# Kernel tuning notes

Measured on AMD Instinct MI355X. Metric: run time of the kernel, lower is better.

Reference implementation:

```python
import jax, jax.numpy as jnp
import numpy as np

N = 100000      # points
M = 12500       # cluster centers
E0 = 1600000    # point-level edges
E1 = 400000     # cluster-level edges
F_IN = 4        # raw point feature dim (e.g. intensity + extras)
D = 64          # hidden feature width
N_CLASSES = 8


def setup_inputs() -> dict:
    key = jax.random.key(0)
    ks = jax.random.split(key, 20)
    s = 0.05
    d = {}
    d["features"] = jax.random.normal(ks[0], (N, F_IN), jnp.float32)
    d["points"] = jax.random.normal(ks[1], (N, 3), jnp.float32)
    d["cluster_centers"] = jax.random.normal(ks[2], (M, 3), jnp.float32)
    d["l0_edges"] = jax.random.randint(ks[3], (E0, 2), 0, N)
    d["l1_edges"] = jax.random.randint(ks[4], (E1, 2), 0, M)
    d["labels"] = jax.random.randint(ks[5], (N,), 0, M)
    # Feature_extract MLP
    d["W_fe"] = s * jax.random.normal(ks[6], (F_IN + 3, D), jnp.float32)
    d["b_fe"] = jnp.zeros((D,), jnp.float32)
    # 4 Mini_GNN layers (layer2, layer2_1, layer6, layer6_1), stacked
    d["mini_We"] = s * jax.random.normal(ks[7], (4, D + 3, D), jnp.float32)
    d["mini_be"] = jnp.zeros((4, D), jnp.float32)
    d["mini_Wu"] = s * jax.random.normal(ks[8], (4, D, D), jnp.float32)
    d["mini_bu"] = jnp.zeros((4, D), jnp.float32)
    # Mini_to_Large
    d["W_m1"] = s * jax.random.normal(ks[9], (D + 3, D), jnp.float32)
    d["b_m1"] = jnp.zeros((D,), jnp.float32)
    d["W_m2"] = s * jax.random.normal(ks[10], (D, D), jnp.float32)
    d["b_m2"] = jnp.zeros((D,), jnp.float32)
    # 2 GNN layers on cluster graph (layer4, layer4_1), stacked
    d["gnn_We"] = s * jax.random.normal(ks[11], (2, D + 3, D), jnp.float32)
    d["gnn_be"] = jnp.zeros((2, D), jnp.float32)
    d["gnn_Wu"] = s * jax.random.normal(ks[12], (2, D, D), jnp.float32)
    d["gnn_bu"] = jnp.zeros((2, D), jnp.float32)
    # Large_to_Mini
    d["W_l"] = s * jax.random.normal(ks[13], (D + 3, D), jnp.float32)
    d["b_l"] = jnp.zeros((D,), jnp.float32)
    # Classifier
    d["W_c"] = s * jax.random.normal(ks[14], (D, N_CLASSES), jnp.float32)
    d["b_c"] = jnp.zeros((N_CLASSES,), jnp.float32)
    return d


def _gnn_layer(feat, pos, edges, We, be, Wu, bu, n_nodes):
    """PointGNN-style layer: gather -> edge MLP -> scatter max -> update MLP -> residual."""
    src, dst = edges[:, 0], edges[:, 1]
    e_in = jnp.concatenate([pos[src] - pos[dst], feat[src]], axis=-1)  # [E, 3+D]
    h = jax.nn.relu(e_in @ We + be)                                     # [E, D]
    agg = jax.ops.segment_max(h, dst, num_segments=n_nodes)            # [n, D]
    agg = jnp.where(jnp.isneginf(agg), 0.0, agg)  # nodes with no in-edges -> 0
    return jax.nn.relu(agg @ Wu + bu) + feat


def reference(features, points, cluster_centers, l0_edges, l1_edges, labels,
              W_fe, b_fe, mini_We, mini_be, mini_Wu, mini_bu,
              W_m1, b_m1, W_m2, b_m2, gnn_We, gnn_be, gnn_Wu, gnn_bu,
              W_l, b_l, W_c, b_c):
    rel = points - cluster_centers[labels]  # [N, 3] point pos relative to its cluster
    # layer1: Feature_extract
    f1 = jax.nn.relu(jnp.concatenate([features, rel], -1) @ W_fe + b_fe)
    # layer2 / layer2_1: Mini_GNN (scatter max) on point graph
    f2 = _gnn_layer(f1, points, l0_edges, mini_We[0], mini_be[0], mini_Wu[0], mini_bu[0], N)
    f2_1 = _gnn_layer(f2, points, l0_edges, mini_We[1], mini_be[1], mini_Wu[1], mini_bu[1], N)
    # layer3: Mini_to_Large (scatter sum by labels)
    h = jax.nn.relu(jnp.concatenate([f2_1, rel], -1) @ W_m1 + b_m1)
    c = jax.ops.segment_sum(h, labels, num_segments=M)  # [M, D]
    f3 = jax.nn.relu(c @ W_m2 + b_m2)
    # layer4 / layer4_1: GNN (scatter max) on cluster graph
    f4 = _gnn_layer(f3, cluster_centers, l1_edges, gnn_We[0], gnn_be[0], gnn_Wu[0], gnn_bu[0], M)
    f4_1 = _gnn_layer(f4, cluster_centers, l1_edges, gnn_We[1], gnn_be[1], gnn_Wu[1], gnn_bu[1], M)
    # layer5: Large_to_Mini (gather by labels)
    f5 = jax.nn.relu(jnp.concatenate([f4_1[labels], rel], -1) @ W_l + b_l)
    # layer6 / layer6_1 with residual skips per call()
    f6 = _gnn_layer(f5, points, l0_edges, mini_We[2], mini_be[2], mini_Wu[2], mini_bu[2], N)
    f6 = f6 + f2_1
    f6_1 = _gnn_layer(f6, points, l0_edges, mini_We[3], mini_be[3], mini_Wu[3], mini_bu[3], N)
    final = f6_1 + f2
    return final @ W_c + b_c  # [N, N_CLASSES] per-point logits
```

## Files before the change

### kernel.cpp

```cpp
#include <hip/hip_runtime.h>

#define N_PTS   100000
#define M_CL    12500
#define E0_N    1600000
#define E1_N    400000

#define NB      256
#define BIN_CAP 32
#define RANGE0  391
#define RANGE1  49
#define BCAP0   8192
#define BCAP1   2048

#define LSTR    72

typedef unsigned short ushortT;
typedef short  short8 __attribute__((ext_vector_type(8)));
typedef float  v4f    __attribute__((ext_vector_type(4)));
typedef _Float16 h2   __attribute__((ext_vector_type(2)));
typedef unsigned u4v  __attribute__((ext_vector_type(4)));

__device__ inline ushortT f2bf(float x){
  union{float f; unsigned u;} v; v.f = x;
  unsigned r = v.u + 0x7fffu + ((v.u >> 16) & 1u);
  return (ushortT)(r >> 16);
}
__device__ inline float bf2f(ushortT h){
  union{unsigned u; float f;} v; v.u = ((unsigned)h) << 16;
  return v.f;
}
__device__ inline ushortT f2h(float x){
  union{_Float16 h; ushortT u;} v; v.h = (_Float16)x;
  return v.u;
}
__device__ inline float h2f(ushortT u){
  union{ushortT u; _Float16 h;} v; v.u = u;
  return (float)v.h;
}
__device__ inline h2 pkmax(h2 a, h2 b){ return __builtin_elementwise_max(a, b); }
__device__ inline h2 u2h(unsigned u){ union{unsigned u; h2 h;} v{u}; return v.h; }


__global__ void k_binit(int* c0, int* c1){
  int t = threadIdx.x;
  c0[t] = t*BCAP0;
  c1[t] = t*BCAP1;
}

template<int RANGE>
__global__ __launch_bounds__(256) void k_bin(const int* __restrict__ edges, int E,
                                             int* __restrict__ bcur, unsigned* __restrict__ tmp){
  __shared__ unsigned stage[NB*BIN_CAP];
  __shared__ int scnt[NB];
  __shared__ int sbase[NB];
  int tid = threadIdx.x;
  int nchunks = (E + 2047) / 2048;
  for (int c = blockIdx.x; c < nchunks; c += gridDim.x){
    int base = c*2048;
    scnt[tid] = 0;
    __syncthreads();
    #pragma unroll
    for (int r=0;r<8;++r){
      int e = base + r*256 + tid;
      if (e < E){
        int s = edges[2*e], d = edges[2*e+1];
        int bk = d / RANGE;
        unsigned packed = ((unsigned)s << 11) | (unsigned)(d - bk*RANGE);
        int pos = atomicAdd(&scnt[bk], 1);
        if (pos < BIN_CAP) stage[bk*BIN_CAP+pos] = packed;
        else tmp[atomicAdd(&bcur[bk],1)] = packed;
      }
    }
    __syncthreads();
    {
      int nfl = scnt[tid]; if (nfl > BIN_CAP) nfl = BIN_CAP;
      sbase[tid] = atomicAdd(&bcur[tid], nfl);
    }
    __syncthreads();
    int wv = tid >> 6, ln = tid & 63;
    for (int bb=0; bb<32; ++bb){
      int bk = wv*64 + bb*2 + (ln>>5);
      int ent = ln & 31;
      int nf = scnt[bk]; if (nf > BIN_CAP) nf = BIN_CAP;
      if (ent < nf) tmp[sbase[bk]+ent] = stage[bk*BIN_CAP+ent];
    }
    __syncthreads();
  }
}

__global__ void k_scan_bases(const int* c0, int* bb0, int* off0e,
                             const int* c1, int* bb1, int* off1e){
  const int* cur = blockIdx.x ? c1 : c0;
  int* bb = blockIdx.x ? bb1 : bb0;
  int* offe = blockIdx.x ? off1e : off0e;
  int BC = blockIdx.x ? BCAP1 : BCAP0;
  int lane = threadIdx.x & 63;
  int base = lane*4;
  int v0 = cur[base+0] - (base+0)*BC;
  int v1 = cur[base+1] - (base+1)*BC;
  int v2 = cur[base+2] - (base+2)*BC;
  int v3 = cur[base+3] - (base+3)*BC;
  int psum = v0+v1+v2+v3, sc = psum;
  #pragma unroll
  for (int st=1; st<64; st<<=1){
    int x = __shfl_up(sc, st, 64);
    if (lane >= st) sc += x;
  }
  int ex = sc - psum;
  bb[base+0] = ex;
  bb[base+1] = ex + v0;
  bb[base+2] = ex + v0 + v1;
  bb[base+3] = ex + v0 + v1 + v2;
  if (lane == 63) *offe = sc;
}

template<int RANGE, int BCAP>
__global__ __launch_bounds__(256) void k_csr_build(const unsigned* __restrict__ tmp, const int* __restrict__ bcur,
                                                   const int* __restrict__ bb, int n,
                                                   int* __restrict__ offs, int* __restrict__ csr){
  constexpr int K = (RANGE + 255) / 256;
  __shared__ int hist[RANGE];
  __shared__ int part[256];
  int b = blockIdx.x, tid = threadIdx.x;
  int dlo = b*RANGE;
  int range = n - dlo; if (range > RANGE) range = RANGE; if (range < 0) range = 0;
  int cnt = bcur[b] - b*BCAP;
  for (int t=tid; t<RANGE; t+=256) hist[t] = 0;
  __syncthreads();
  const unsigned* sl = tmp + (size_t)b*BCAP;
  for (int j=tid; j<cnt; j+=256) atomicAdd(&hist[sl[j] & 2047u], 1);
  __syncthreads();
  int s = 0; int loc[K];
  #pragma unroll
  for (int kk=0; kk<K; ++kk){
    int idx = tid*K + kk;
    int v = (idx < RANGE) ? hist[idx] : 0;
    loc[kk] = s; s += v;
  }
  part[tid] = s; __syncthreads();
  int own = s;
  for (int st=1; st<256; st<<=1){
    int x = (tid >= st) ? part[tid-st] : 0;
    __syncthreads();
    part[tid] += x;
    __syncthreads();
  }
  int ebase = part[tid] - own;
  int gb = bb[b];
  __syncthreads();
  #pragma unroll
  for (int kk=0; kk<K; ++kk){
    int idx = tid*K + kk;
    if (idx < RANGE){
      int ex = ebase + loc[kk];
      if (idx < range) offs[dlo+idx] = gb + ex;
      hist[idx] = ex;
    }
  }
  __syncthreads();
  for (int j=tid; j<cnt; j+=256){
    unsigned p = sl[j];
    int pos = atomicAdd(&hist[p & 2047u], 1);
    csr[gb + pos] = (int)(p >> 11);
  }
}


__global__ __launch_bounds__(256) void k_count_lab(const int* __restrict__ labels, int n, int* __restrict__ cnt){
  int i = blockIdx.x*256 + threadIdx.x;
  if (i < n) atomicAdd(&cnt[labels[i]], 1);
}

__global__ __launch_bounds__(256) void k_chunk_sum(const int* __restrict__ cnt, int n, int* __restrict__ part){
  __shared__ int sd[256];
  int t = threadIdx.x, base = blockIdx.x*2048;
  int s = 0;
  #pragma unroll
  for (int r=0;r<8;++r){ int i = base + t*8 + r; if (i<n) s += cnt[i]; }
  sd[t]=s; __syncthreads();
  for (int st=128; st>0; st>>=1){ if (t<st) sd[t]+=sd[t+st]; __syncthreads(); }
  if (t==0) part[blockIdx.x]=sd[0];
}

__global__ void k_scan_part(int* part, int B, int* offs, int n){
  int lane = threadIdx.x & 63;
  int v = (lane < B) ? part[lane] : 0;
  int orig = v;
  #pragma unroll
  for (int st=1; st<64; st<<=1){
    int x = __shfl_up(v, st, 64);
    if (lane >= st) v += x;
  }
  if (lane < B) part[lane] = v - orig;
  if (lane == 63) offs[n] = v;
}

__global__ __launch_bounds__(256) void k_chunk_scan(const int* __restrict__ cnt, int n,
                                                    const int* __restrict__ part, int* __restrict__ offs){
  __shared__ int sd[256];
  int t=threadIdx.x, base=blockIdx.x*2048;
  int v[8]; int s=0;
  #pragma unroll
  for (int r=0;r<8;++r){ int i=base+t*8+r; v[r] = (i<n)?cnt[i]:0; s+=v[r]; }
  sd[t]=s; __syncthreads();
  for (int st=1; st<256; st<<=1){
    int x = (t>=st)? sd[t-st] : 0;
    __syncthreads();
    sd[t]+=x;
    __syncthreads();
  }
  int acc = part[blockIdx.x] + sd[t] - s;
  #pragma unroll
  for (int r=0;r<8;++r){ int i=base+t*8+r; if (i<n) offs[i]=acc; acc+=v[r]; }
}

__global__ __launch_bounds__(256) void k_fill_lab(const int* __restrict__ labels, int n,
                                                  const int* __restrict__ offs, int* __restrict__ cur,
                                                  int* __restrict__ csr){
  int i = blockIdx.x*256 + threadIdx.x;
  if (i < n){
    int d = labels[i];
    int p = atomicAdd(&cur[d], 1);
    csr[offs[d]+p] = i;
  }
}


struct WSrc { const float* p[16]; };

__global__ __launch_bounds__(256) void k_wprep(WSrc s, ushortT* __restrict__ wt, ushortT* __restrict__ wtc){
  int slot = blockIdx.x;
  if (slot < 15){
    const float* src = s.p[slot];
    ushortT* dst = wt + slot*4096;
    for (int e=threadIdx.x; e<4096; e+=256){
      int nn = e>>6, kk = e&63;
      dst[e] = f2bf(src[kk*64+nn]);
    }
  } else {
    const float* src = s.p[15];
    for (int e=threadIdx.x; e<1024; e+=256){
      int nn = e>>6, kk = e&63;
      wtc[e] = (nn<8) ? f2bf(src[kk*8+nn]) : (ushortT)0;
    }
  }
}


__global__ __launch_bounds__(256) void k_f1g(const float* __restrict__ features, const float* __restrict__ points,
                                             const float* __restrict__ centers, const int* __restrict__ labels,
                                             const float* __restrict__ W, const float* __restrict__ b,
                                             const ushortT* __restrict__ Wt2, const float* __restrict__ bias2,
                                             const float* __restrict__ Wr2,
                                             float* __restrict__ rel, ushortT* __restrict__ f1b,
                                             ushortT* __restrict__ gout, int n, int ntiles){
  __shared__ ushortT lds[4*16*LSTR];
  int tid = threadIdx.x;
  int lane = tid & 63, wslot = tid >> 6;
  int quad = lane >> 4, l15 = lane & 15;
  int gw = (blockIdx.x*256 + tid) >> 6;
  int nw = (gridDim.x*256) >> 6;
  float Wf0=W[0*64+lane], Wf1=W[1*64+lane], Wf2=W[2*64+lane], Wf3=W[3*64+lane];
  float wr0=W[4*64+lane], wr1=W[5*64+lane], wr2=W[6*64+lane];
  float bias=b[lane];
  short8 s0_0 = *(const short8*)(Wt2 + ( 0 + l15)*64 +  0 + quad*8);
  short8 s0_1 = *(const short8*)(Wt2 + ( 0 + l15)*64 + 32 + quad*8);
  short8 s1_0 = *(const short8*)(Wt2 + (16 + l15)*64 +  0 + quad*8);
  short8 s1_1 = *(const short8*)(Wt2 + (16 + l15)*64 + 32 + quad*8);
  short8 s2_0 = *(const short8*)(Wt2 + (32 + l15)*64 +  0 + quad*8);
  short8 s2_1 = *(const short8*)(Wt2 + (32 + l15)*64 + 32 + quad*8);
  short8 s3_0 = *(const short8*)(Wt2 + (48 + l15)*64 +  0 + quad*8);
  short8 s3_1 = *(const short8*)(Wt2 + (48 + l15)*64 + 32 + quad*8);
  float eb0 = bias2[l15], eb1 = bias2[16+l15], eb2 = bias2[32+l15], eb3 = bias2[48+l15];
  float e0c0=Wr2[0*64+l15], e0c1=Wr2[0*64+16+l15], e0c2=Wr2[0*64+32+l15], e0c3=Wr2[0*64+48+l15];
  float e1c0=Wr2[1*64+l15], e1c1=Wr2[1*64+16+l15], e1c2=Wr2[1*64+32+l15], e1c3=Wr2[1*64+48+l15];
  float e2c0=Wr2[2*64+l15], e2c1=Wr2[2*64+16+l15], e2c2=Wr2[2*64+32+l15], e2c3=Wr2[2*64+48+l15];

  for (int t=gw; t<ntiles; t+=nw){
    int i0 = t*16;
    for (int r=0;r<16;++r){
      int row = i0 + r;
      bool ok = row < n;
      int rr = ok ? row : n-1;
      int lb = labels[rr];
      float rx = points[rr*3+0]-centers[lb*3+0];
      float ry = points[rr*3+1]-centers[lb*3+1];
      float rz = points[rr*3+2]-centers[lb*3+2];
      float acc = bias + wr0*rx + wr1*ry + wr2*rz;
      acc += features[rr*4+0]*Wf0 + features[rr*4+1]*Wf1;
      acc += features[rr*4+2]*Wf2 + features[rr*4+3]*Wf3;
      acc = fmaxf(acc, 0.f);
      ushortT ab = f2bf(acc);
      if (ok){
        f1b[(size_t)row*64+lane] = ab;
        if (lane==0){ rel[row*3+0]=rx; rel[row*3+1]=ry; rel[row*3+2]=rz; }
      }
      lds[wslot*(16*LSTR) + r*LSTR + lane] = ab;
    }
    __builtin_amdgcn_wave_barrier();
    const ushortT* lp = lds + wslot*(16*LSTR) + l15*LSTR + quad*8;
    short8 sa0 = *(const short8*)(lp);
    short8 sa1 = *(const short8*)(lp + 32);
    __builtin_amdgcn_wave_barrier();
    v4f ec0 = {0.f,0.f,0.f,0.f}, ec1 = ec0, ec2 = ec0, ec3 = ec0;
    ec0 = __builtin_amdgcn_mfma_f32_16x16x32_bf16(sa0, s0_0, ec0, 0,0,0);
    ec1 = __builtin_amdgcn_mfma_f32_16x16x32_bf16(sa0, s1_0, ec1, 0,0,0);
    ec2 = __builtin_amdgcn_mfma_f32_16x16x32_bf16(sa0, s2_0, ec2, 0,0,0);
    ec3 = __builtin_amdgcn_mfma_f32_16x16x32_bf16(sa0, s3_0, ec3, 0,0,0);
    ec0 = __builtin_amdgcn_mfma_f32_16x16x32_bf16(sa1, s0_1, ec0, 0,0,0);
    ec1 = __builtin_amdgcn_mfma_f32_16x16x32_bf16(sa1, s1_1, ec1, 0,0,0);
    ec2 = __builtin_amdgcn_mfma_f32_16x16x32_bf16(sa1, s2_1, ec2, 0,0,0);
    ec3 = __builtin_amdgcn_mfma_f32_16x16x32_bf16(sa1, s3_1, ec3, 0,0,0);
    #pragma unroll
    for (int r=0;r<4;++r){
      int row = i0 + quad*4 + r;
      if (row < n){
        float vx=points[row*3+0], vy=points[row*3+1], vz=points[row*3+2];
        float g0 = ec0[r] + eb0 + vx*e0c0 + vy*e1c0 + vz*e2c0;
        float g1 = ec1[r] + eb1 + vx*e0c1 + vy*e1c1 + vz*e2c1;
        float g2 = ec2[r] + eb2 + vx*e0c2 + vy*e1c2 + vz*e2c2;
        float g3 = ec3[r] + eb3 + vx*e0c3 + vy*e1c3 + vz*e2c3;
        size_t base = (size_t)row*64 + l15;
        gout[base] = f2h(g0); gout[base+16] = f2h(g1); gout[base+32] = f2h(g2); gout[base+48] = f2h(g3);
      }
    }
  }
}


template<bool RELU, int NRES, bool USEREL, bool GATHER, bool OUT16, bool F16O, int EMODE, bool ERELU>
__global__ __launch_bounds__(256) void k_gemm(
    const ushortT* __restrict__ A, const ushortT* __restrict__ Wt,
    const float* __restrict__ bias, const float* __restrict__ Wr,
    const float* __restrict__ rel, const int* __restrict__ gidx,
    const ushortT* __restrict__ r1, const ushortT* __restrict__ r2,
    ushortT* __restrict__ out16,
    const ushortT* __restrict__ Wt2, const float* __restrict__ bias2,
    const float* __restrict__ Wr2, const float* __restrict__ vec2,
    void* __restrict__ eout,
    int n, int ntiles)
{
  constexpr int LDSZ = (EMODE>0) ? 4*16*LSTR : 4;
  __shared__ ushortT lds[LDSZ];
  int tid = threadIdx.x;
  int lane = tid & 63, wslot = tid >> 6;
  int quad = lane >> 4, l15 = lane & 15;
  int gw = (blockIdx.x*256 + tid) >> 6;
  int nw = (gridDim.x*256) >> 6;

  short8 bfr0_0 = *(const short8*)(Wt + ( 0 + l15)*64 +  0 + quad*8);
  short8 bfr0_1 = *(const short8*)(Wt + ( 0 + l15)*64 + 32 + quad*8);
  short8 bfr1_0 = *(const short8*)(Wt + (16 + l15)*64 +  0 + quad*8);
  short8 bfr1_1 = *(const short8*)(Wt + (16 + l15)*64 + 32 + quad*8);
  short8 bfr2_0 = *(const short8*)(Wt + (32 + l15)*64 +  0 + quad*8);
  short8 bfr2_1 = *(const short8*)(Wt + (32 + l15)*64 + 32 + quad*8);
  short8 bfr3_0 = *(const short8*)(Wt + (48 + l15)*64 +  0 + quad*8);
  short8 bfr3_1 = *(const short8*)(Wt + (48 + l15)*64 + 32 + quad*8);
  float bs0 = bias[ 0 + l15], bs1 = bias[16 + l15];
  float bs2 = bias[32 + l15], bs3 = bias[48 + l15];
  float w0c0=0,w0c1=0,w0c2=0,w0c3=0, w1c0=0,w1c1=0,w1c2=0,w1c3=0, w2c0=0,w2c1=0,w2c2=0,w2c3=0;
  if (USEREL){
    w0c0=Wr[0*64+l15]; w0c1=Wr[0*64+16+l15]; w0c2=Wr[0*64+32+l15]; w0c3=Wr[0*64+48+l15];
    w1c0=Wr[1*64+l15]; w1c1=Wr[1*64+16+l15]; w1c2=Wr[1*64+32+l15]; w1c3=Wr[1*64+48+l15];
    w2c0=Wr[2*64+l15]; w2c1=Wr[2*64+16+l15]; w2c2=Wr[2*64+32+l15]; w2c3=Wr[2*64+48+l15];
  }

  short8 s0_0{}, s0_1{}, s1_0{}, s1_1{}, s2_0{}, s2_1{}, s3_0{}, s3_1{};
  float eb0=0, eb1=0, eb2=0, eb3=0;
  float e0c0=0,e0c1=0,e0c2=0,e0c3=0, e1c0=0,e1c1=0,e1c2=0,e1c3=0, e2c0=0,e2c1=0,e2c2=0,e2c3=0;
  float ebias_c = 0.f;
  if (EMODE == 1){
    s0_0 = *(const short8*)(Wt2 + ( 0 + l15)*64 +  0 + quad*8);
    s0_1 = *(const short8*)(Wt2 + ( 0 + l15)*64 + 32 + quad*8);
    s1_0 = *(const short8*)(Wt2 + (16 + l15)*64 +  0 + quad*8);
    s1_1 = *(const short8*)(Wt2 + (16 + l15)*64 + 32 + quad*8);
    s2_0 = *(const short8*)(Wt2 + (32 + l15)*64 +  0 + quad*8);
    s2_1 = *(const short8*)(Wt2 + (32 + l15)*64 + 32 + quad*8);
    s3_0 = *(const short8*)(Wt2 + (48 + l15)*64 +  0 + quad*8);
    s3_1 = *(const short8*)(Wt2 + (48 + l15)*64 + 32 + quad*8);
    eb0 = bias2[l15]; eb1 = bias2[16+l15]; eb2 = bias2[32+l15]; eb3 = bias2[48+l15];
    e0c0=Wr2[0*64+l15]; e0c1=Wr2[0*64+16+l15]; e0c2=Wr2[0*64+32+l15]; e0c3=Wr2[0*64+48+l15];
    e1c0=Wr2[1*64+l15]; e1c1=Wr2[1*64+16+l15]; e1c2=Wr2[1*64+32+l15]; e1c3=Wr2[1*64+48+l15];
    e2c0=Wr2[2*64+l15]; e2c1=Wr2[2*64+16+l15]; e2c2=Wr2[2*64+32+l15]; e2c3=Wr2[2*64+48+l15];
  } else if (EMODE == 2){
    s0_0 = *(const short8*)(Wt2 + l15*64 +  0 + quad*8);
    s0_1 = *(const short8*)(Wt2 + l15*64 + 32 + quad*8);
    ebias_c = (l15 < 8) ? bias2[l15] : 0.f;
  }

  for (int t=gw; t<ntiles; t+=nw){
    int i0 = t*16;
    int rowA = i0 + l15; if (rowA >= n) rowA = n-1;
    if (GATHER) rowA = gidx[rowA];
    const ushortT* ap = A + (size_t)rowA*64 + quad*8;
    short8 a0 = *(const short8*)(ap);
    short8 a1 = *(const short8*)(ap + 32);
    v4f ac0 = {0.f,0.f,0.f,0.f}, ac1 = ac0, ac2 = ac0, ac3 = ac0;
    ac0 = __builtin_amdgcn_mfma_f32_16x16x32_bf16(a0, bfr0_0, ac0, 0,0,0);
    ac1 = __builtin_amdgcn_mfma_f32_16x16x32_bf16(a0, bfr1_0, ac1, 0,0,0);
    ac2 = __builtin_amdgcn_mfma_f32_16x16x32_bf16(a0, bfr2_0, ac2, 0,0,0);
    ac3 = __builtin_amdgcn_mfma_f32_16x16x32_bf16(a0, bfr3_0, ac3, 0,0,0);
    ac0 = __builtin_amdgcn_mfma_f32_16x16x32_bf16(a1, bfr0_1, ac0, 0,0,0);
    ac1 = __builtin_amdgcn_mfma_f32_16x16x32_bf16(a1, bfr1_1, ac1, 0,0,0);
    ac2 = __builtin_amdgcn_mfma_f32_16x16x32_bf16(a1, bfr2_1, ac2, 0,0,0);
    ac3 = __builtin_amdgcn_mfma_f32_16x16x32_bf16(a1, bfr3_1, ac3, 0,0,0);

    #pragma unroll
    for (int r=0;r<4;++r){
      int row = i0 + quad*4 + r;
      bool rowok = (row < n);
      float rx=0.f, ry=0.f, rz=0.f;
      if (USEREL && rowok){ rx=rel[row*3+0]; ry=rel[row*3+1]; rz=rel[row*3+2]; }
      float v0 = ac0[r] + bs0, v1 = ac1[r] + bs1, v2 = ac2[r] + bs2, v3 = ac3[r] + bs3;
      if (USEREL){
        v0 += rx*w0c0 + ry*w1c0 + rz*w2c0;
        v1 += rx*w0c1 + ry*w1c1 + rz*w2c1;
        v2 += rx*w0c2 + ry*w1c2 + rz*w2c2;
        v3 += rx*w0c3 + ry*w1c3 + rz*w2c3;
      }
      if (RELU){ v0=fmaxf(v0,0.f); v1=fmaxf(v1,0.f); v2=fmaxf(v2,0.f); v3=fmaxf(v3,0.f); }
      size_t base = (size_t)row*64 + l15;
      if (rowok){
        if (NRES>=1){
          v0 += bf2f(r1[base]); v1 += bf2f(r1[base+16]); v2 += bf2f(r1[base+32]); v3 += bf2f(r1[base+48]);
        }
        if (NRES>=2){
          v0 += bf2f(r2[base]); v1 += bf2f(r2[base+16]); v2 += bf2f(r2[base+32]); v3 += bf2f(r2[base+48]);
        }
        if (OUT16){
          if (F16O){
            out16[base] = f2h(v0); out16[base+16] = f2h(v1); out16[base+32] = f2h(v2); out16[base+48] = f2h(v3);
          } else {
            out16[base] = f2bf(v0); out16[base+16] = f2bf(v1); out16[base+32] = f2bf(v2); out16[base+48] = f2bf(v3);
          }
        }
      }
      if (EMODE > 0){
        int lb = wslot*(16*LSTR) + (quad*4+r)*LSTR + l15;
        lds[lb]      = f2bf(v0);
        lds[lb + 16] = f2bf(v1);
        lds[lb + 32] = f2bf(v2);
        lds[lb + 48] = f2bf(v3);
      }
    }

    if (EMODE > 0){
      __builtin_amdgcn_wave_barrier();
      const ushortT* lp = lds + wslot*(16*LSTR) + l15*LSTR + quad*8;
      short8 sa0 = *(const short8*)(lp);
      short8 sa1 = *(const short8*)(lp + 32);
      __builtin_amdgcn_wave_barrier();
      if (EMODE == 1){
        v4f ec0 = {0.f,0.f,0.f,0.f}, ec1 = ec0, ec2 = ec0, ec3 = ec0;
        ec0 = __builtin_amdgcn_mfma_f32_16x16x32_bf16(sa0, s0_0, ec0, 0,0,0);
        ec1 = __builtin_amdgcn_mfma_f32_16x16x32_bf16(sa0, s1_0, ec1, 0,0,0);
        ec2 = __builtin_amdgcn_mfma_f32_16x16x32_bf16(sa0, s2_0, ec2, 0,0,0);
        ec3 = __builtin_amdgcn_mfma_f32_16x16x32_bf16(sa0, s3_0, ec3, 0,0,0);
        ec0 = __builtin_amdgcn_mfma_f32_16x16x32_bf16(sa1, s0_1, ec0, 0,0,0);
        ec1 = __builtin_amdgcn_mfma_f32_16x16x32_bf16(sa1, s1_1, ec1, 0,0,0);
        ec2 = __builtin_amdgcn_mfma_f32_16x16x32_bf16(sa1, s2_1, ec2, 0,0,0);
        ec3 = __builtin_amdgcn_mfma_f32_16x16x32_bf16(sa1, s3_1, ec3, 0,0,0);
        ushortT* eo = (ushortT*)eout;
        #pragma unroll
        for (int r=0;r<4;++r){
          int row = i0 + quad*4 + r;
          if (row < n){
            float vx=vec2[row*3+0], vy=vec2[row*3+1], vz=vec2[row*3+2];
            float g0 = ec0[r] + eb0 + vx*e0c0 + vy*e1c0 + vz*e2c0;
            float g1 = ec1[r] + eb1 + vx*e0c1 + vy*e1c1 + vz*e2c1;
            float g2 = ec2[r] + eb2 + vx*e0c2 + vy*e1c2 + vz*e2c2;
            float g3 = ec3[r] + eb3 + vx*e0c3 + vy*e1c3 + vz*e2c3;
            if (ERELU){ g0=fmaxf(g0,0.f); g1=fmaxf(g1,0.f); g2=fmaxf(g2,0.f); g3=fmaxf(g3,0.f); }
            size_t base = (size_t)row*64 + l15;
            eo[base] = f2h(g0); eo[base+16] = f2h(g1); eo[base+32] = f2h(g2); eo[base+48] = f2h(g3);
          }
        }
      } else {
        v4f ec = {0.f,0.f,0.f,0.f};
        ec = __builtin_amdgcn_mfma_f32_16x16x32_bf16(sa0, s0_0, ec, 0,0,0);
        ec = __builtin_amdgcn_mfma_f32_16x16x32_bf16(sa1, s0_1, ec, 0,0,0);
        if (l15 < 8){
          float* eo = (float*)eout;
          #pragma unroll
          for (int r=0;r<4;++r){
            int row = i0 + quad*4 + r;
            if (row < n) eo[(size_t)row*8 + l15] = ec[r] + ebias_c;
          }
        }
      }
    }
  }
}


__global__ __launch_bounds__(256) void k_edge_agg(const int* __restrict__ offs, const int* __restrict__ csr,
                                                  const float* __restrict__ pos, const ushortT* __restrict__ g,
                                                  const float* __restrict__ Wp, ushortT* __restrict__ agg, int n){
  int lane = threadIdx.x & 63;
  int grp = lane >> 3, d8 = lane & 7;
  int gbase = lane & 56;
  int gw = (blockIdx.x*256 + threadIdx.x) >> 6;
  int nw = (gridDim.x*256) >> 6;
  const u4v* g4 = (const u4v*)g;
  float2 w0[4], w1[4], w2[4];
  #pragma unroll
  for (int q=0;q<4;++q){
    w0[q] = *(const float2*)(Wp + 0*64 + d8*8 + 2*q);
    w1[q] = *(const float2*)(Wp + 1*64 + d8*8 + 2*q);
    w2[q] = *(const float2*)(Wp + 2*64 + d8*8 + 2*q);
  }
  const h2 NEGBIG = {(_Float16)-60000.f, (_Float16)-60000.f};
  int n8 = (n+7) >> 3;
  for (int ii=gw; ii<n8; ii+=nw){
    int i0 = ii*8;
    int ig = i0 + grp; bool ok = ig < n; if (!ok) ig = n-1;
    int b = offs[ig], e = offs[ig+1];
    int cnt = e - b, c1 = cnt - 1;
    int mx = cnt;
    mx = max(mx, __shfl_xor(mx, 8, 64));
    mx = max(mx, __shfl_xor(mx, 16, 64));
    mx = max(mx, __shfl_xor(mx, 32, 64));
    h2 m0=NEGBIG, m1=NEGBIG, m2=NEGBIG, m3=NEGBIG;
    for (int J=0; J<mx; J+=8){
      if (J < cnt){
        int sv = csr[b + min(J + d8, c1)];
        #pragma unroll
        for (int jj=0; jj<8; ++jj){
          int s = __shfl(sv, gbase + jj, 64);
          u4v u = g4[(size_t)s*8 + d8];
          m0 = pkmax(m0, u2h(u.x));
          m1 = pkmax(m1, u2h(u.y));
          m2 = pkmax(m2, u2h(u.z));
          m3 = pkmax(m3, u2h(u.w));
        }
      }
    }
    float px = pos[ig*3+0], py = pos[ig*3+1], pz = pos[ig*3+2];
    u4v outv;
    {
      float sA = w0[0].x*px + w1[0].x*py + w2[0].x*pz;
      float sB = w0[0].y*px + w1[0].y*py + w2[0].y*pz;
      float x0 = fmaxf((float)m0.x - sA, 0.f);
      float x1 = fmaxf((float)m0.y - sB, 0.f);
      outv.x = (unsigned)f2bf(x0) | ((unsigned)f2bf(x1) << 16);
    }
    {
      float sA = w0[1].x*px + w1[1].x*py + w2[1].x*pz;
      float sB = w0[1].y*px + w1[1].y*py + w2[1].y*pz;
      float x0 = fmaxf((float)m1.x - sA, 0.f);
      float x1 = fmaxf((float)m1.y - sB, 0.f);
      outv.y = (unsigned)f2bf(x0) | ((unsigned)f2bf(x1) << 16);
    }
    {
      float sA = w0[2].x*px + w1[2].x*py + w2[2].x*pz;
      float sB = w0[2].y*px + w1[2].y*py + w2[2].y*pz;
      float x0 = fmaxf((float)m2.x - sA, 0.f);
      float x1 = fmaxf((float)m2.y - sB, 0.f);
      outv.z = (unsigned)f2bf(x0) | ((unsigned)f2bf(x1) << 16);
    }
    {
      float sA = w0[3].x*px + w1[3].x*py + w2[3].x*pz;
      float sB = w0[3].y*px + w1[3].y*py + w2[3].y*pz;
      float x0 = fmaxf((float)m3.x - sA, 0.f);
      float x1 = fmaxf((float)m3.y - sB, 0.f);
      outv.w = (unsigned)f2bf(x0) | ((unsigned)f2bf(x1) << 16);
    }
    if (ok) ((u4v*)agg)[(size_t)ig*8 + d8] = outv;
  }
}


__global__ __launch_bounds__(256) void k_seg_gather(const int* __restrict__ offs, const int* __restrict__ csr,
                                                    const ushortT* __restrict__ h, ushortT* __restrict__ c, int m){
  int lane = threadIdx.x & 63;
  int wv = (blockIdx.x*256 + threadIdx.x) >> 6;
  if (wv >= m) return;
  int b = offs[wv], e = offs[wv+1];
  float acc = 0.f;
  for (int k=b; k<e; ++k){
    int i = csr[k];
    acc += h2f(h[(size_t)i*64+lane]);
  }
  c[(size_t)wv*64+lane] = f2bf(acc);
}


extern "C" void kernel_launch(void* const* d_in, const int* in_sizes, int n_in,
                              void* d_out, int out_size, void* d_ws, size_t ws_size,
                              hipStream_t stream){
  const float* features = (const float*)d_in[0];
  const float* points   = (const float*)d_in[1];
  const float* centers  = (const float*)d_in[2];
  const int*   l0e      = (const int*)d_in[3];
  const int*   l1e      = (const int*)d_in[4];
  const int*   labels   = (const int*)d_in[5];
  const float* W_fe = (const float*)d_in[6];
  const float* b_fe = (const float*)d_in[7];
  const float* mWe  = (const float*)d_in[8];
  const float* mbe  = (const float*)d_in[9];
  const float* mWu  = (const float*)d_in[10];
  const float* mbu  = (const float*)d_in[11];
  const float* W_m1 = (const float*)d_in[12];
  const float* b_m1 = (const float*)d_in[13];
  const float* W_m2 = (const float*)d_in[14];
  const float* b_m2 = (const float*)d_in[15];
  const float* gWe  = (const float*)d_in[16];
  const float* gbe  = (const float*)d_in[17];
  const float* gWu  = (const float*)d_in[18];
  const float* gbu  = (const float*)d_in[19];
  const float* W_l  = (const float*)d_in[20];
  const float* b_l  = (const float*)d_in[21];
  const float* W_c  = (const float*)d_in[22];
  const float* b_c  = (const float*)d_in[23];
  float* out = (float*)d_out;

  char* w = (char*)d_ws;
  size_t off = 0;
  auto alloc = [&](size_t bytes)->void*{
    void* p = (void*)(w + off);
    off = (off + bytes + 255) & ~(size_t)255;
    return p;
  };
  float* rel  = (float*)alloc((size_t)N_PTS*3*4);
  ushortT* UF1 = (ushortT*)alloc((size_t)N_PTS*64*2);
  ushortT* UF2 = (ushortT*)alloc((size_t)N_PTS*64*2);
  ushortT* UF21= (ushortT*)alloc((size_t)N_PTS*64*2);
  ushortT* UF5 = (ushortT*)alloc((size_t)N_PTS*64*2);
  ushortT* UF6 = (ushortT*)alloc((size_t)N_PTS*64*2);
  ushortT* gbuf= (ushortT*)alloc((size_t)N_PTS*64*2);
  ushortT* abuf= (ushortT*)alloc((size_t)N_PTS*64*2);
  ushortT* cb_b= (ushortT*)alloc((size_t)M_CL*64*2);
  ushortT* UF3 = (ushortT*)alloc((size_t)M_CL*64*2);
  ushortT* UF4 = (ushortT*)alloc((size_t)M_CL*64*2);
  ushortT* cg_b= (ushortT*)alloc((size_t)M_CL*64*2);
  ushortT* cagg_b = (ushortT*)alloc((size_t)M_CL*64*2);
  ushortT* f41_b  = (ushortT*)alloc((size_t)M_CL*64*2);
  ushortT* wt  = (ushortT*)alloc((size_t)15*4096*2);
  ushortT* wtc = (ushortT*)alloc((size_t)1024*2);
  int* offs0 = (int*)alloc((size_t)(N_PTS+1)*4);
  int* csr0  = (int*)alloc((size_t)E0_N*4);
  int* offs1 = (int*)alloc((size_t)(M_CL+1)*4);
  int* csr1  = (int*)alloc((size_t)E1_N*4);
  unsigned* tmp0 = (unsigned*)alloc((size_t)NB*BCAP0*4);
  unsigned* tmp1 = (unsigned*)alloc((size_t)NB*BCAP1*4);
  int* bcur0 = (int*)alloc(NB*4);
  int* bcur1 = (int*)alloc(NB*4);
  int* bb0   = (int*)alloc(NB*4);
  int* bb1   = (int*)alloc(NB*4);
  char* zbase = (char*)alloc(0);
  int* cntL = (int*)alloc((size_t)M_CL*4);
  int* curL = (int*)alloc((size_t)M_CL*4);
  size_t zbytes = (size_t)((char*)(w+off) - zbase);
  int* offsL = (int*)alloc((size_t)(M_CL+1)*4);
  int* csrL  = (int*)alloc((size_t)N_PTS*4);
  int* partL = (int*)alloc(64*4);
  (void)ws_size; (void)in_sizes; (void)n_in; (void)out_size;

  const int NT_N = (N_PTS+15)/16;
  const int NT_M = (M_CL +15)/16;
  const int GBG_N = 1563;
  const int GBG_M = 196;
  const int GB_N  = 2048;

  hipMemsetAsync(zbase, 0, zbytes, stream);

  k_binit<<<1, 256, 0, stream>>>(bcur0, bcur1);
  k_bin<RANGE0><<<256, 256, 0, stream>>>(l0e, E0_N, bcur0, tmp0);
  k_bin<RANGE1><<<196, 256, 0, stream>>>(l1e, E1_N, bcur1, tmp1);
  k_scan_bases<<<2, 64, 0, stream>>>(bcur0, bb0, offs0+N_PTS, bcur1, bb1, offs1+M_CL);
  k_csr_build<RANGE0,BCAP0><<<NB, 256, 0, stream>>>(tmp0, bcur0, bb0, N_PTS, offs0, csr0);
  k_csr_build<RANGE1,BCAP1><<<NB, 256, 0, stream>>>(tmp1, bcur1, bb1, M_CL, offs1, csr1);

  k_count_lab<<<(N_PTS+255)/256, 256, 0, stream>>>(labels, N_PTS, cntL);
  k_chunk_sum<<<7, 256, 0, stream>>>(cntL, M_CL, partL);
  k_scan_part<<<1, 64, 0, stream>>>(partL, 7, offsL, M_CL);
  k_chunk_scan<<<7, 256, 0, stream>>>(cntL, M_CL, partL, offsL);
  k_fill_lab<<<(N_PTS+255)/256, 256, 0, stream>>>(labels, N_PTS, offsL, curL, csrL);

  WSrc ws{};
  ws.p[0]=mWu+0*4096; ws.p[1]=mWu+1*4096; ws.p[2]=mWu+2*4096; ws.p[3]=mWu+3*4096;
  ws.p[4]=W_m2; ws.p[5]=gWu+0*4096; ws.p[6]=gWu+1*4096;
  ws.p[7]=mWe+0*4288+192; ws.p[8]=mWe+1*4288+192; ws.p[9]=mWe+2*4288+192; ws.p[10]=mWe+3*4288+192;
  ws.p[11]=W_m1; ws.p[12]=W_l; ws.p[13]=gWe+0*4288+192; ws.p[14]=gWe+1*4288+192;
  ws.p[15]=W_c;
  k_wprep<<<16, 256, 0, stream>>>(ws, wt, wtc);

  k_f1g<<<GBG_N, 256, 0, stream>>>(features, points, centers, labels, W_fe, b_fe,
      wt+7*4096, mbe+0, mWe+0*4288, rel, UF1, gbuf, N_PTS, NT_N);

  k_edge_agg<<<GB_N,256,0,stream>>>(offs0, csr0, points, gbuf, mWe+0*4288, abuf, N_PTS);
  k_gemm<true,1,false,false,true,false,1,false><<<GBG_N,256,0,stream>>>(abuf, wt+0*4096, mbu+0,
      nullptr, nullptr, nullptr, UF1, nullptr, UF2,
      wt+8*4096, mbe+64, mWe+1*4288, points, gbuf, N_PTS, NT_N);
  k_edge_agg<<<GB_N,256,0,stream>>>(offs0, csr0, points, gbuf, mWe+1*4288, abuf, N_PTS);
  k_gemm<true,1,false,false,true,false,1,true><<<GBG_N,256,0,stream>>>(abuf, wt+1*4096, mbu+64,
      nullptr, nullptr, nullptr, UF2, nullptr, UF21,
      wt+11*4096, b_m1, W_m1+4096, rel, gbuf, N_PTS, NT_N);
  k_seg_gather<<<(M_CL*64+255)/256, 256, 0, stream>>>(offsL, csrL, gbuf, cb_b, M_CL);
  k_gemm<true,0,false,false,true,false,1,false><<<GBG_M,256,0,stream>>>(cb_b, wt+4*4096, b_m2,
      nullptr, nullptr, nullptr, nullptr, nullptr, UF3,
      wt+13*4096, gbe+0, gWe+0*4288, centers, cg_b, M_CL, NT_M);
  k_edge_agg<<<GBG_M,256,0,stream>>>(offs1, csr1, centers, cg_b, gWe+0*4288, cagg_b, M_CL);
  k_gemm<true,1,false,false,true,false,1,false><<<GBG_M,256,0,stream>>>(cagg_b, wt+5*4096, gbu+0,
      nullptr, nullptr, nullptr, UF3, nullptr, UF4,
      wt+14*4096, gbe+64, gWe+1*4288, centers, cg_b, M_CL, NT_M);
  k_edge_agg<<<GBG_M,256,0,stream>>>(offs1, csr1, centers, cg_b, gWe+1*4288, cagg_b, M_CL);
  k_gemm<true,1,false,false,true,false,0,false><<<GBG_M,256,0,stream>>>(cagg_b, wt+6*4096, gbu+64,
      nullptr, nullptr, nullptr, UF4, nullptr, f41_b,
      nullptr, nullptr, nullptr, nullptr, nullptr, M_CL, NT_M);
  k_gemm<true,0,true,true,true,false,1,false><<<GBG_N,256,0,stream>>>(f41_b, wt+12*4096, b_l,
      W_l+4096, rel, labels, nullptr, nullptr, UF5,
      wt+9*4096, mbe+128, mWe+2*4288, points, gbuf, N_PTS, NT_N);
  k_edge_agg<<<GB_N,256,0,stream>>>(offs0, csr0, points, gbuf, mWe+2*4288, abuf, N_PTS);
  k_gemm<true,2,false,false,true,false,1,false><<<GBG_N,256,0,stream>>>(abuf, wt+2*4096, mbu+128,
      nullptr, nullptr, nullptr, UF5, UF21, UF6,
      wt+10*4096, mbe+192, mWe+3*4288, points, gbuf, N_PTS, NT_N);
  k_edge_agg<<<GB_N,256,0,stream>>>(offs0, csr0, points, gbuf, mWe+3*4288, abuf, N_PTS);
  k_gemm<true,2,false,false,false,false,2,false><<<GBG_N,256,0,stream>>>(abuf, wt+3*4096, mbu+192,
      nullptr, nullptr, nullptr, UF6, UF2, nullptr,
      wtc, b_c, nullptr, nullptr, out, N_PTS, NT_N);
}
```

Measured before the change: 526.2 us.

## Fuse edge max-aggregation into the following update GEMM kernel

Removes the standalone edge aggregation kernel and performs the CSR gather/max over neighbour edge features inside the update GEMM, staging the 16-row aggregate tile through LDS before the MFMA. Since the GEMM also writes the next layer's edge-transformed features, the gather buffers are now double-buffered (gA/gB, cgA/cgB) to avoid read/write hazards. This drops a round trip of the aggregate buffer through global memory and several launches. In exchange, the gather loop runs at the GEMM's grid size and occupancy rather than its own tuned grid, and uses more registers and LDS.

```diff
diff --git a/kernel.cpp b/kernel.cpp
--- a/kernel.cpp
+++ b/kernel.cpp
@@ -328,7 +328,7 @@
 }
 
 
-template<bool RELU, int NRES, bool USEREL, bool GATHER, bool OUT16, bool F16O, int EMODE, bool ERELU>
+template<bool RELU, int NRES, bool USEREL, bool GATHER, bool OUT16, bool F16O, int EMODE, bool ERELU, bool AGGIN>
 __global__ __launch_bounds__(256) void k_gemm(
     const ushortT* __restrict__ A, const ushortT* __restrict__ Wt,
     const float* __restrict__ bias, const float* __restrict__ Wr,
@@ -338,9 +338,12 @@
     const ushortT* __restrict__ Wt2, const float* __restrict__ bias2,
     const float* __restrict__ Wr2, const float* __restrict__ vec2,
     void* __restrict__ eout,
+    const int* __restrict__ aoffs, const int* __restrict__ acsr,
+    const float* __restrict__ apos, const float* __restrict__ aWp,
+    const ushortT* __restrict__ aG,
     int n, int ntiles)
 {
-  constexpr int LDSZ = (EMODE>0) ? 4*16*LSTR : 4;
+  constexpr int LDSZ = (EMODE>0 || AGGIN) ? 4*16*LSTR : 4;
   __shared__ ushortT lds[LDSZ];
   int tid = threadIdx.x;
   int lane = tid & 63, wslot = tid >> 6;
@@ -364,6 +367,19 @@
     w1c0=Wr[1*64+l15]; w1c1=Wr[1*64+16+l15]; w1c2=Wr[1*64+32+l15]; w1c3=Wr[1*64+48+l15];
     w2c0=Wr[2*64+l15]; w2c1=Wr[2*64+16+l15]; w2c2=Wr[2*64+32+l15]; w2c3=Wr[2*64+48+l15];
   }
+
+  int grp = lane >> 3, d8 = lane & 7, gbase = lane & 56;
+  const u4v* g4 = (const u4v*)aG;
+  float2 aw0[4], aw1[4], aw2[4];
+  if (AGGIN){
+    #pragma unroll
+    for (int q=0;q<4;++q){
+      aw0[q] = *(const float2*)(aWp + 0*64 + d8*8 + 2*q);
+      aw1[q] = *(const float2*)(aWp + 1*64 + d8*8 + 2*q);
+      aw2[q] = *(const float2*)(aWp + 2*64 + d8*8 + 2*q);
+    }
+  }
+  const h2 NEGBIG = {(_Float16)-60000.f, (_Float16)-60000.f};
 
   short8 s0_0{}, s0_1{}, s1_0{}, s1_1{}, s2_0{}, s2_1{}, s3_0{}, s3_1{};
   float eb0=0, eb1=0, eb2=0, eb3=0;
@@ -390,11 +406,73 @@
 
   for (int t=gw; t<ntiles; t+=nw){
     int i0 = t*16;
-    int rowA = i0 + l15; if (rowA >= n) rowA = n-1;
-    if (GATHER) rowA = gidx[rowA];
-    const ushortT* ap = A + (size_t)rowA*64 + quad*8;
-    short8 a0 = *(const short8*)(ap);
-    short8 a1 = *(const short8*)(ap + 32);
+    short8 a0, a1;
+    if (AGGIN){
+      #pragma unroll
+      for (int p=0;p<2;++p){
+        int ig = i0 + p*8 + grp;
+        int igc = (ig < n) ? ig : n-1;
+        int b = aoffs[igc], e = aoffs[igc+1];
+        int cnt = e - b, c1 = cnt - 1;
+        int mx = cnt;
+        mx = max(mx, __shfl_xor(mx, 8, 64));
+        mx = max(mx, __shfl_xor(mx, 16, 64));
+        mx = max(mx, __shfl_xor(mx, 32, 64));
+        h2 m0=NEGBIG, m1=NEGBIG, m2=NEGBIG, m3=NEGBIG;
+        for (int J=0; J<mx; J+=8){
+          if (J < cnt){
+            int sv = acsr[b + min(J + d8, c1)];
+            #pragma unroll
+            for (int jj=0; jj<8; ++jj){
+              int s = __shfl(sv, gbase + jj, 64);
+              u4v u = g4[(size_t)s*8 + d8];
+              m0 = pkmax(m0, u2h(u.x));
+              m1 = pkmax(m1, u2h(u.y));
+              m2 = pkmax(m2, u2h(u.z));
+              m3 = pkmax(m3, u2h(u.w));
+            }
+          }
+        }
+        float px = apos[igc*3+0], py = apos[igc*3+1], pz = apos[igc*3+2];
+        u4v outv;
+        {
+          float sA = aw0[0].x*px + aw1[0].x*py + aw2[0].x*pz;
+          float sB = aw0[0].y*px + aw1[0].y*py + aw2[0].y*pz;
+          outv.x = (unsigned)f2bf(fmaxf((float)m0.x - sA, 0.f)) |
+                   ((unsigned)f2bf(fmaxf((float)m0.y - sB, 0.f)) << 16);
+        }
+        {
+          float sA = aw0[1].x*px + aw1[1].x*py + aw2[1].x*pz;
+          float sB = aw0[1].y*px + aw1[1].y*py + aw2[1].y*pz;
+          outv.y = (unsigned)f2bf(fmaxf((float)m1.x - sA, 0.f)) |
+                   ((unsigned)f2bf(fmaxf((float)m1.y - sB, 0.f)) << 16);
+        }
+        {
+          float sA = aw0[2].x*px + aw1[2].x*py + aw2[2].x*pz;
+          float sB = aw0[2].y*px + aw1[2].y*py + aw2[2].y*pz;
+          outv.z = (unsigned)f2bf(fmaxf((float)m2.x - sA, 0.f)) |
+                   ((unsigned)f2bf(fmaxf((float)m2.y - sB, 0.f)) << 16);
+        }
+        {
+          float sA = aw0[3].x*px + aw1[3].x*py + aw2[3].x*pz;
+          float sB = aw0[3].y*px + aw1[3].y*py + aw2[3].y*pz;
+          outv.w = (unsigned)f2bf(fmaxf((float)m3.x - sA, 0.f)) |
+                   ((unsigned)f2bf(fmaxf((float)m3.y - sB, 0.f)) << 16);
+        }
+        *(u4v*)(lds + wslot*(16*LSTR) + (p*8+grp)*LSTR + d8*8) = outv;
+      }
+      __builtin_amdgcn_wave_barrier();
+      const ushortT* lpa = lds + wslot*(16*LSTR) + l15*LSTR + quad*8;
+      a0 = *(const short8*)(lpa);
+      a1 = *(const short8*)(lpa + 32);
+      __builtin_amdgcn_wave_barrier();
+    } else {
+      int rowA = i0 + l15; if (rowA >= n) rowA = n-1;
+      if (GATHER) rowA = gidx[rowA];
+      const ushortT* ap = A + (size_t)rowA*64 + quad*8;
+      a0 = *(const short8*)(ap);
+      a1 = *(const short8*)(ap + 32);
+    }
     v4f ac0 = {0.f,0.f,0.f,0.f}, ac1 = ac0, ac2 = ac0, ac3 = ac0;
     ac0 = __builtin_amdgcn_mfma_f32_16x16x32_bf16(a0, bfr0_0, ac0, 0,0,0);
     ac1 = __builtin_amdgcn_mfma_f32_16x16x32_bf16(a0, bfr1_0, ac1, 0,0,0);
@@ -493,83 +571,6 @@
 }
 
 
-__global__ __launch_bounds__(256) void k_edge_agg(const int* __restrict__ offs, const int* __restrict__ csr,
-                                                  const float* __restrict__ pos, const ushortT* __restrict__ g,
-                                                  const float* __restrict__ Wp, ushortT* __restrict__ agg, int n){
-  int lane = threadIdx.x & 63;
-  int grp = lane >> 3, d8 = lane & 7;
-  int gbase = lane & 56;
-  int gw = (blockIdx.x*256 + threadIdx.x) >> 6;
-  int nw = (gridDim.x*256) >> 6;
-  const u4v* g4 = (const u4v*)g;
-  float2 w0[4], w1[4], w2[4];
-  #pragma unroll
-  for (int q=0;q<4;++q){
-    w0[q] = *(const float2*)(Wp + 0*64 + d8*8 + 2*q);
-    w1[q] = *(const float2*)(Wp + 1*64 + d8*8 + 2*q);
-    w2[q] = *(const float2*)(Wp + 2*64 + d8*8 + 2*q);
-  }
-  const h2 NEGBIG = {(_Float16)-60000.f, (_Float16)-60000.f};
-  int n8 = (n+7) >> 3;
-  for (int ii=gw; ii<n8; ii+=nw){
-    int i0 = ii*8;
-    int ig = i0 + grp; bool ok = ig < n; if (!ok) ig = n-1;
-    int b = offs[ig], e = offs[ig+1];
-    int cnt = e - b, c1 = cnt - 1;
-    int mx = cnt;
-    mx = max(mx, __shfl_xor(mx, 8, 64));
-    mx = max(mx, __shfl_xor(mx, 16, 64));
-    mx = max(mx, __shfl_xor(mx, 32, 64));
-    h2 m0=NEGBIG, m1=NEGBIG, m2=NEGBIG, m3=NEGBIG;
-    for (int J=0; J<mx; J+=8){
-      if (J < cnt){
-        int sv = csr[b + min(J + d8, c1)];
-        #pragma unroll
-        for (int jj=0; jj<8; ++jj){
-          int s = __shfl(sv, gbase + jj, 64);
-          u4v u = g4[(size_t)s*8 + d8];
-          m0 = pkmax(m0, u2h(u.x));
-          m1 = pkmax(m1, u2h(u.y));
-          m2 = pkmax(m2, u2h(u.z));
-          m3 = pkmax(m3, u2h(u.w));
-        }
-      }
-    }
-    float px = pos[ig*3+0], py = pos[ig*3+1], pz = pos[ig*3+2];
-    u4v outv;
-    {
-      float sA = w0[0].x*px + w1[0].x*py + w2[0].x*pz;
-      float sB = w0[0].y*px + w1[0].y*py + w2[0].y*pz;
-      float x0 = fmaxf((float)m0.x - sA, 0.f);
-      float x1 = fmaxf((float)m0.y - sB, 0.f);
-      outv.x = (unsigned)f2bf(x0) | ((unsigned)f2bf(x1) << 16);
-    }
-    {
-      float sA = w0[1].x*px + w1[1].x*py + w2[1].x*pz;
-      float sB = w0[1].y*px + w1[1].y*py + w2[1].y*pz;
-      float x0 = fmaxf((float)m1.x - sA, 0.f);
-      float x1 = fmaxf((float)m1.y - sB, 0.f);
-      outv.y = (unsigned)f2bf(x0) | ((unsigned)f2bf(x1) << 16);
-    }
-    {
-      float sA = w0[2].x*px + w1[2].x*py + w2[2].x*pz;
-      float sB = w0[2].y*px + w1[2].y*py + w2[2].y*pz;
-      float x0 = fmaxf((float)m2.x - sA, 0.f);
-      float x1 = fmaxf((float)m2.y - sB, 0.f);
-      outv.z = (unsigned)f2bf(x0) | ((unsigned)f2bf(x1) << 16);
-    }
-    {
-      float sA = w0[3].x*px + w1[3].x*py + w2[3].x*pz;
-      float sB = w0[3].y*px + w1[3].y*py + w2[3].y*pz;
-      float x0 = fmaxf((float)m3.x - sA, 0.f);
-      float x1 = fmaxf((float)m3.y - sB, 0.f);
-      outv.w = (unsigned)f2bf(x0) | ((unsigned)f2bf(x1) << 16);
-    }
-    if (ok) ((u4v*)agg)[(size_t)ig*8 + d8] = outv;
-  }
-}
-
-
 __global__ __launch_bounds__(256) void k_seg_gather(const int* __restrict__ offs, const int* __restrict__ csr,
                                                     const ushortT* __restrict__ h, ushortT* __restrict__ c, int m){
   int lane = threadIdx.x & 63;
@@ -627,13 +628,13 @@
   ushortT* UF21= (ushortT*)alloc((size_t)N_PTS*64*2);
   ushortT* UF5 = (ushortT*)alloc((size_t)N_PTS*64*2);
   ushortT* UF6 = (ushortT*)alloc((size_t)N_PTS*64*2);
-  ushortT* gbuf= (ushortT*)alloc((size_t)N_PTS*64*2);
-  ushortT* abuf= (ushortT*)alloc((size_t)N_PTS*64*2);
+  ushortT* gA  = (ushortT*)alloc((size_t)N_PTS*64*2);
+  ushortT* gB  = (ushortT*)alloc((size_t)N_PTS*64*2);
   ushortT* cb_b= (ushortT*)alloc((size_t)M_CL*64*2);
   ushortT* UF3 = (ushortT*)alloc((size_t)M_CL*64*2);
   ushortT* UF4 = (ushortT*)alloc((size_t)M_CL*64*2);
-  ushortT* cg_b= (ushortT*)alloc((size_t)M_CL*64*2);
-  ushortT* cagg_b = (ushortT*)alloc((size_t)M_CL*64*2);
+  ushortT* cgA = (ushortT*)alloc((size_t)M_CL*64*2);
+  ushortT* cgB = (ushortT*)alloc((size_t)M_CL*64*2);
   ushortT* f41_b  = (ushortT*)alloc((size_t)M_CL*64*2);
   ushortT* wt  = (ushortT*)alloc((size_t)15*4096*2);
   ushortT* wtc = (ushortT*)alloc((size_t)1024*2);
@@ -660,7 +661,6 @@
   const int NT_M = (M_CL +15)/16;
   const int GBG_N = 1563;
   const int GBG_M = 196;
-  const int GB_N  = 2048;
 
   hipMemsetAsync(zbase, 0, zbytes, stream);
 
@@ -686,37 +686,39 @@
   k_wprep<<<16, 256, 0, stream>>>(ws, wt, wtc);
 
   k_f1g<<<GBG_N, 256, 0, stream>>>(features, points, centers, labels, W_fe, b_fe,
-      wt+7*4096, mbe+0, mWe+0*4288, rel, UF1, gbuf, N_PTS, NT_N);
-
-  k_edge_agg<<<GB_N,256,0,stream>>>(offs0, csr0, points, gbuf, mWe+0*4288, abuf, N_PTS);
-  k_gemm<true,1,false,false,true,false,1,false><<<GBG_N,256,0,stream>>>(abuf, wt+0*4096, mbu+0,
+      wt+7*4096, mbe+0, mWe+0*4288, rel, UF1, gA, N_PTS, NT_N);
+
+  k_gemm<true,1,false,false,true,false,1,false,true><<<GBG_N,256,0,stream>>>(nullptr, wt+0*4096, mbu+0,
       nullptr, nullptr, nullptr, UF1, nullptr, UF2,
-      wt+8*4096, mbe+64, mWe+1*4288, points, gbuf, N_PTS, NT_N);
-  k_edge_agg<<<GB_N,256,0,stream>>>(offs0, csr0, points, gbuf, mWe+1*4288, abuf, N_PTS);
-  k_gemm<true,1,false,false,true,false,1,true><<<GBG_N,256,0,stream>>>(abuf, wt+1*4096, mbu+64,
+      wt+8*4096, mbe+64, mWe+1*4288, points, gB,
+      offs0, csr0, points, mWe+0*4288, gA, N_PTS, NT_N);
+  k_gemm<true,1,false,false,true,false,1,true,true><<<GBG_N,256,0,stream>>>(nullptr, wt+1*4096, mbu+64,
       nullptr, nullptr, nullptr, UF2, nullptr, UF21,
-      wt+11*4096, b_m1, W_m1+4096, rel, gbuf, N_PTS, NT_N);
-  k_seg_gather<<<(M_CL*64+255)/256, 256, 0, stream>>>(offsL, csrL, gbuf, cb_b, M_CL);
-  k_gemm<true,0,false,false,true,false,1,false><<<GBG_M,256,0,stream>>>(cb_b, wt+4*4096, b_m2,
+      wt+11*4096, b_m1, W_m1+4096, rel, gA,
+      offs0, csr0, points, mWe+1*4288, gB, N_PTS, NT_N);
+  k_seg_gather<<<(M_CL*64+255)/256, 256, 0, stream>>>(offsL, csrL, gA, cb_b, M_CL);
+  k_gemm<true,0,false,false,true,false,1,false,false><<<GBG_M,256,0,stream>>>(cb_b, wt+4*4096, b_m2,
       nullptr, nullptr, nullptr, nullptr, nullptr, UF3,
-      wt+13*4096, gbe+0, gWe+0*4288, centers, cg_b, M_CL, NT_M);
-  k_edge_agg<<<GBG_M,256,0,stream>>>(offs1, csr1, centers, cg_b, gWe+0*4288, cagg_b, M_CL);
-  k_gemm<true,1,false,false,true,false,1,false><<<GBG_M,256,0,stream>>>(cagg_b, wt+5*4096, gbu+0,
+      wt+13*4096, gbe+0, gWe+0*4288, centers, cgA,
+      nullptr, nullptr, nullptr, nullptr, nullptr, M_CL, NT_M);
+  k_gemm<true,1,false,false,true,false,1,false,true><<<GBG_M,256,0,stream>>>(nullptr, wt+5*4096, gbu+0,
       nullptr, nullptr, nullptr, UF3, nullptr, UF4,
-      wt+14*4096, gbe+64, gWe+1*4288, centers, cg_b, M_CL, NT_M);
-  k_edge_agg<<<GBG_M,256,0,stream>>>(offs1, csr1, centers, cg_b, gWe+1*4288, cagg_b, M_CL);
-  k_gemm<true,1,false,false,true,false,0,false><<<GBG_M,256,0,stream>>>(cagg_b, wt+6*4096, gbu+64,
+      wt+14*4096, gbe+64, gWe+1*4288, centers, cgB,
+      offs1, csr1, centers, gWe+0*4288, cgA, M_CL, NT_M);
+  k_gemm<true,1,false,false,true,false,0,false,true><<<GBG_M,256,0,stream>>>(nullptr, wt+6*4096, gbu+64,
       nullptr, nullptr, nullptr, UF4, nullptr, f41_b,
-      nullptr, nullptr, nullptr, nullptr, nullptr, M_CL, NT_M);
-  k_gemm<true,0,true,true,true,false,1,false><<<GBG_N,256,0,stream>>>(f41_b, wt+12*4096, b_l,
+      nullptr, nullptr, nullptr, nullptr, nullptr,
+      offs1, csr1, centers, gWe+1*4288, cgB, M_CL, NT_M);
+  k_gemm<true,0,true,true,true,false,1,false,false><<<GBG_N,256,0,stream>>>(f41_b, wt+12*4096, b_l,
       W_l+4096, rel, labels, nullptr, nullptr, UF5,
-      wt+9*4096, mbe+128, mWe+2*4288, points, gbuf, N_PTS, NT_N);
-  k_edge_agg<<<GB_N,256,0,stream>>>(offs0, csr0, points, gbuf, mWe+2*4288, abuf, N_PTS);
-  k_gemm<true,2,false,false,true,false,1,false><<<GBG_N,256,0,stream>>>(abuf, wt+2*4096, mbu+128,
+      wt+9*4096, mbe+128, mWe+2*4288, points, gB,
+      nullptr, nullptr, nullptr, nullptr, nullptr, N_PTS, NT_N);
+  k_gemm<true,2,false,false,true,false,1,false,true><<<GBG_N,256,0,stream>>>(nullptr, wt+2*4096, mbu+128,
       nullptr, nullptr, nullptr, UF5, UF21, UF6,
-      wt+10*4096, mbe+192, mWe+3*4288, points, gbuf, N_PTS, NT_N);
-  k_edge_agg<<<GB_N,256,0,stream>>>(offs0, csr0, points, gbuf, mWe+3*4288, abuf, N_PTS);
-  k_gemm<true,2,false,false,false,false,2,false><<<GBG_N,256,0,stream>>>(abuf, wt+3*4096, mbu+192,
+      wt+10*4096, mbe+192, mWe+3*4288, points, gA,
+      offs0, csr0, points, mWe+2*4288, gB, N_PTS, NT_N);
+  k_gemm<true,2,false,false,false,false,2,false,true><<<GBG_N,256,0,stream>>>(nullptr, wt+3*4096, mbu+192,
       nullptr, nullptr, nullptr, UF6, UF2, nullptr,
-      wtc, b_c, nullptr, nullptr, out, N_PTS, NT_N);
-}
+      wtc, b_c, nullptr, nullptr, out,
+      offs0, csr0, points, mWe+3*4288, gA, N_PTS, NT_N);
+}
```

New measurement: 754.2 us. 1.43x slower.
